# Kernel tuning notes

Measured on AMD Instinct MI355X. Metric: run time of the kernel, lower is better.

## Reference

```python
import jax, jax.numpy as jnp
import numpy as np
from jax import lax

X_SIZE, Z_SIZE, H, GC, PD = 256, 64, 64, 16, 2
B, K, T = 256, 16, 50
LOG_SIG_MIN, LOG_SIG_MAX, LOG_P_MAX = -10.0, 10.0, 50.0
ZX = X_SIZE + Z_SIZE
LSTM_IN = ZX + PD


def setup_inputs() -> dict:
    key = jax.random.key(0)
    ks = jax.random.split(key, 24)
    s = lambda fan_in: 1.0 / np.sqrt(fan_in)
    u = lambda k, shape, sc: jax.random.uniform(k, shape, jnp.float32, -sc, sc)
    inp = {
        'x': jax.random.normal(ks[0], (B, X_SIZE), jnp.float32),
        'z_stacked': jax.random.normal(ks[1], (K, B, Z_SIZE), jnp.float32),
        'input_seqs': jax.random.normal(ks[2], (B, 8, 2, 2, 6), jnp.float32),
        'pred_seqs': jax.random.normal(ks[3], (B, T, 2, 2, 6), jnp.float32),
        # initial_h / initial_c linears: ZX -> H
        'Wh0': u(ks[4], (H, ZX), s(ZX)), 'bh0': u(ks[5], (H,), s(ZX)),
        'Wc0': u(ks[6], (H, ZX), s(ZX)), 'bc0': u(ks[7], (H,), s(ZX)),
        # LSTMCell: gates order i,f,g,o
        'Wih': u(ks[8], (4 * H, LSTM_IN), s(H)), 'Whh': u(ks[9], (4 * H, H), s(H)),
        'bih': u(ks[10], (4 * H,), s(H)), 'bhh': u(ks[11], (4 * H,), s(H)),
        # GMM parameter heads: H -> GC / GC*PD
        'Wpi': u(ks[12], (GC, H), s(H)), 'bpi': u(ks[13], (GC,), s(H)),
        'Wmu': u(ks[14], (GC * PD, H), s(H)), 'bmu': u(ks[15], (GC * PD,), s(H)),
        'Wls': u(ks[16], (GC * PD, H), s(H)), 'bls': u(ks[17], (GC * PD,), s(H)),
        'Wcorr': u(ks[18], (GC, H), s(H)), 'bcorr': u(ks[19], (GC,), s(H)),
        'n_z_samples': K,
    }
    return inp


def _gmm2d_log_prob(log_pis, mus, log_sigmas, corrs, value):
    # log_pis/corrs: [K,B,T,GC]; mus/log_sigmas: [K,B,T,GC*PD]; value: [B,T,PD]
    ls = jnp.clip(log_sigmas, LOG_SIG_MIN, LOG_SIG_MAX).reshape(K, B, T, GC, PD)
    mu = mus.reshape(K, B, T, GC, PD)
    dx = value[None, :, :, None, :] - mu                      # [K,B,T,GC,PD]
    zscore = dx * jnp.exp(-ls)                                # dx / sigma
    one_m_rho2 = 1.0 - corrs ** 2
    quad = (zscore[..., 0] ** 2 + zscore[..., 1] ** 2
            - 2.0 * corrs * zscore[..., 0] * zscore[..., 1])
    comp = (-jnp.log(2.0 * jnp.pi) - ls.sum(-1)
            - 0.5 * jnp.log(one_m_rho2) - 0.5 * quad / one_m_rho2)
    log_pi_n = jax.nn.log_softmax(log_pis, axis=-1)
    log_p_t = jax.nn.logsumexp(log_pi_n + comp, axis=-1)      # [K,B,T]
    return jnp.minimum(log_p_t, LOG_P_MAX)


def reference(x, z_stacked, input_seqs, pred_seqs,
              Wh0, bh0, Wc0, bc0, Wih, Whh, bih, bhh,
              Wpi, bpi, Wmu, bmu, Wls, bls, Wcorr, bcorr, n_z_samples):
    tgt_future = pred_seqs[:, :, 1, 1, 2:4]                   # [B,T,2]
    tgt_present = input_seqs[:, -1, 1, 1, 2:4]                # [B,2]
    z = z_stacked.reshape(-1, z_stacked.shape[-1])            # [K*B, z]
    zx = jnp.concatenate([z, jnp.tile(x, (n_z_samples, 1))], axis=1)  # [N, ZX]
    N = zx.shape[0]
    h0 = zx @ Wh0.T + bh0
    c0 = zx @ Wc0.T + bc0
    decode_inputs = jnp.concatenate([tgt_present[:, None, :], tgt_future[:, :T - 1, :]], axis=1)  # [B,T,2]
    inputs = jnp.concatenate([
        jnp.broadcast_to(zx[:, None, :], (N, T, ZX)),
        jnp.tile(decode_inputs, (n_z_samples, 1, 1))], axis=2)  # [N,T,ZX+2]

    def step(carry, xt):
        h, c = carry
        gates = xt @ Wih.T + bih + h @ Whh.T + bhh
        i, f, g, o = jnp.split(gates, 4, axis=-1)
        c = jax.nn.sigmoid(f) * c + jax.nn.sigmoid(i) * jnp.tanh(g)
        h = jax.nn.sigmoid(o) * jnp.tanh(c)
        return (h, c), h

    _, hs = lax.scan(step, (h0, c0), jnp.swapaxes(inputs, 0, 1))  # [T,N,H]
    hs = jnp.swapaxes(hs, 0, 1)                                   # [N,T,H]

    log_pis = (hs @ Wpi.T + bpi).reshape(K, B, T, GC)
    mus = (hs @ Wmu.T + bmu).reshape(K, B, T, GC * PD)
    log_sigmas = (hs @ Wls.T + bls).reshape(K, B, T, GC * PD)
    corrs = jnp.tanh(hs @ Wcorr.T + bcorr).reshape(K, B, T, GC)

    log_p_yt_xz = _gmm2d_log_prob(log_pis, mus, log_sigmas, corrs, tgt_future)
    return log_p_yt_xz.sum(axis=2)                                # [K,B]
```

## Files before the change

### kernel.cpp

```cpp
#include <hip/hip_runtime.h>


#define T_ 50
#define SPB 16
#define ZXS 324
#define HFS 72
#define GLS 256
#define PLS 100

typedef __attribute__((ext_vector_type(8))) short short8;
typedef __attribute__((ext_vector_type(4))) float f32x4;

#define MFMA(a, b, c) __builtin_amdgcn_mfma_f32_16x16x32_bf16(a, b, c, 0, 0, 0)

__device__ __forceinline__ float sigf(float x)  { return 1.0f / (1.0f + __expf(-x)); }
__device__ __forceinline__ float tanh_(float x) { return 1.0f - 2.0f / (__expf(2.0f * x) + 1.0f); }

__device__ __forceinline__ void splitf(float f, unsigned short& hi, unsigned short& lo) {
    unsigned b = __float_as_uint(f);
    hi = (unsigned short)(b >> 16);
    float fh = __uint_as_float(b & 0xffff0000u);
    lo = (unsigned short)(__float_as_uint(f - fh) >> 16);
}

__device__ __forceinline__ void pack8(const float* p, short8& hi, short8& lo) {
    #pragma unroll
    for (int e = 0; e < 8; ++e) {
        unsigned short h, l;
        splitf(p[e], h, l);
        hi[e] = (short)h; lo[e] = (short)l;
    }
}

__launch_bounds__(512, 2)
__global__ void decoder_kernel(
    const float* __restrict__ x,       const float* __restrict__ z,
    const float* __restrict__ inp_seqs,const float* __restrict__ pred_seqs,
    const float* __restrict__ Wh0,     const float* __restrict__ bh0,
    const float* __restrict__ Wc0,     const float* __restrict__ bc0,
    const float* __restrict__ Wih,     const float* __restrict__ Whh,
    const float* __restrict__ bih,     const float* __restrict__ bhh,
    const float* __restrict__ Wpi,     const float* __restrict__ bpi,
    const float* __restrict__ Wmu,     const float* __restrict__ bmu,
    const float* __restrict__ Wls,     const float* __restrict__ bls,
    const float* __restrict__ Wcorr,   const float* __restrict__ bcorr,
    float* __restrict__ out)
{
    __shared__ __align__(16) float smem[9504];
    float* ZXL = smem;
    float* GL  = smem;
    float* PL  = smem + 4096;
    float* C0X = smem + 5696;
    unsigned short* HFhi = (unsigned short*)(smem + 6720);
    unsigned short* HFlo = (unsigned short*)(smem + 7296);
    float* FUT = smem + 7872;
    float* PRS = smem + 9472;

    const int j = threadIdx.x;
    const int w = j >> 6;
    const int l = j & 63;
    const int g = l >> 4;
    const int c = l & 15;
    const int blk = blockIdx.x;

    for (int e = j; e < SPB*320; e += 512) {
        int s = e / 320, k = e - s*320;
        int n = blk*SPB + s; int kk = n >> 8; int b = n & 255;
        ZXL[s*ZXS + k] = (k < 64) ? z[(kk*256 + b)*64 + k] : x[b*256 + (k - 64)];
    }
    for (int e = j; e < T_*SPB; e += 512) {
        int t = e >> 4, s = e & 15;
        int b = (blk*SPB + s) & 255;
        float2 v = *reinterpret_cast<const float2*>(pred_seqs + b*1200 + t*24 + 20);
        FUT[t*32 + s*2] = v.x; FUT[t*32 + s*2 + 1] = v.y;
    }
    if (j < SPB) {
        int b = (blk*SPB + j) & 255;
        float2 v = *reinterpret_cast<const float2*>(inp_seqs + b*192 + 188);
        PRS[j*2] = v.x; PRS[j*2 + 1] = v.y;
    }
    __syncthreads();

    const int gate0 = w*32 + c;
    const int gate1 = w*32 + 16 + c;
    const int colB  = w*16 + c;

    f32x4 gc0, gc1, accB;
    {
        float bA0 = bih[gate0] + bhh[gate0];
        float bA1 = bih[gate1] + bhh[gate1];
        float bB  = (w < 4) ? bh0[colB] : bc0[colB - 64];
        gc0 = (f32x4){bA0, bA0, bA0, bA0};
        gc1 = (f32x4){bA1, bA1, bA1, bA1};
        accB = (f32x4){bB, bB, bB, bB};
    }
    const float* rowA0 = Wih + gate0*322;
    const float* rowA1 = Wih + gate1*322;
    const float* rowB  = (w < 4) ? (Wh0 + colB*320) : (Wc0 + (colB - 64)*320);

    for (int ks = 0; ks < 10; ++ks) {
        int k0 = ks*32 + g*8;
        short8 ahi, alo, b0h, b0l, b1h, b1l, bbh, bbl;
        pack8(&ZXL[c*ZXS + k0], ahi, alo);
        pack8(rowA0 + k0, b0h, b0l);
        pack8(rowA1 + k0, b1h, b1l);
        pack8(rowB  + k0, bbh, bbl);
        gc0  = MFMA(ahi, b0h, gc0);  gc0  = MFMA(ahi, b0l, gc0);  gc0  = MFMA(alo, b0h, gc0);
        gc1  = MFMA(ahi, b1h, gc1);  gc1  = MFMA(ahi, b1l, gc1);  gc1  = MFMA(alo, b1h, gc1);
        accB = MFMA(ahi, bbh, accB); accB = MFMA(ahi, bbl, accB); accB = MFMA(alo, bbh, accB);
    }

    if (w < 4) {
        #pragma unroll
        for (int r = 0; r < 4; ++r) {
            int s = g*4 + r;
            unsigned short hh, ll; splitf(accB[r], hh, ll);
            HFhi[s*HFS + colB] = hh; HFlo[s*HFS + colB] = ll;
        }
    } else {
        #pragma unroll
        for (int r = 0; r < 4; ++r) C0X[(g*4 + r)*64 + (colB - 64)] = accB[r];
    }

    const float wd00 = rowA0[320], wd01 = rowA0[321];
    const float wd10 = rowA1[320], wd11 = rowA1[321];
    short8 w1h00, w1l00, w1h01, w1l01, w1h10, w1l10, w1h11, w1l11;
    pack8(Whh + gate0*64 +      g*8, w1h00, w1l00);
    pack8(Whh + gate0*64 + 32 + g*8, w1h01, w1l01);
    pack8(Whh + gate1*64 +      g*8, w1h10, w1l10);
    pack8(Whh + gate1*64 + 32 + g*8, w1h11, w1l11);

    short8 b3h0, b3l0, b3h1, b3l1;
    float bias3;
    {
        int r3 = (w < 6) ? (w*16 + c) : 0;
        const float* prow; float bb;
        if (r3 < 16)      { prow = Wpi   + r3*64;       bb = bpi[r3]; }
        else if (r3 < 48) { prow = Wmu   + (r3-16)*64;  bb = bmu[r3-16]; }
        else if (r3 < 80) { prow = Wls   + (r3-48)*64;  bb = bls[r3-48]; }
        else              { prow = Wcorr + (r3-80)*64;  bb = bcorr[r3-80]; }
        bias3 = bb;
        pack8(prow +      g*8, b3h0, b3l0);
        pack8(prow + 32 + g*8, b3h1, b3l1);
    }

    __syncthreads();

    const int u2 = j & 63, sg2 = j >> 6;
    float cst0 = C0X[(2*sg2 + 0)*64 + u2];
    float cst1 = C0X[(2*sg2 + 1)*64 + u2];

    const int s3 = j >> 4, g3 = j & 15;
    float sum = 0.0f;

    for (int t = 0; t < T_; ++t) {
        {
            const float* dptr = (t == 0) ? PRS : &FUT[(t-1)*32];
            f32x4 a0, a1;
            #pragma unroll
            for (int r = 0; r < 4; ++r) {
                float2 dv = *reinterpret_cast<const float2*>(dptr + (g*4 + r)*2);
                a0[r] = gc0[r] + dv.x*wd00 + dv.y*wd01;
                a1[r] = gc1[r] + dv.x*wd10 + dv.y*wd11;
            }
            short8 ah0 = *reinterpret_cast<const short8*>(HFhi + c*HFS +      g*8);
            short8 al0 = *reinterpret_cast<const short8*>(HFlo + c*HFS +      g*8);
            short8 ah1 = *reinterpret_cast<const short8*>(HFhi + c*HFS + 32 + g*8);
            short8 al1 = *reinterpret_cast<const short8*>(HFlo + c*HFS + 32 + g*8);
            a0 = MFMA(ah0, w1h00, a0); a0 = MFMA(ah0, w1l00, a0); a0 = MFMA(al0, w1h00, a0);
            a0 = MFMA(ah1, w1h01, a0); a0 = MFMA(ah1, w1l01, a0); a0 = MFMA(al1, w1h01, a0);
            a1 = MFMA(ah0, w1h10, a1); a1 = MFMA(ah0, w1l10, a1); a1 = MFMA(al0, w1h10, a1);
            a1 = MFMA(ah1, w1h11, a1); a1 = MFMA(ah1, w1l11, a1); a1 = MFMA(al1, w1h11, a1);
            #pragma unroll
            for (int r = 0; r < 4; ++r) {
                GL[(g*4 + r)*GLS + gate0] = a0[r];
                GL[(g*4 + r)*GLS + gate1] = a1[r];
            }
        }
        __syncthreads();

        {
            #pragma unroll
            for (int i = 0; i < 2; ++i) {
                int s = 2*sg2 + i;
                float gi = GL[s*GLS + u2];
                float gf = GL[s*GLS + 64  + u2];
                float gg = GL[s*GLS + 128 + u2];
                float go = GL[s*GLS + 192 + u2];
                float cp = (i == 0) ? cst0 : cst1;
                float cc = sigf(gf)*cp + sigf(gi)*tanh_(gg);
                if (i == 0) cst0 = cc; else cst1 = cc;
                float hh = sigf(go)*tanh_(cc);
                unsigned short uh, ul; splitf(hh, uh, ul);
                HFhi[s*HFS + u2] = uh; HFlo[s*HFS + u2] = ul;
            }
        }
        __syncthreads();

        if (w < 6) {
            short8 ah0 = *reinterpret_cast<const short8*>(HFhi + c*HFS +      g*8);
            short8 al0 = *reinterpret_cast<const short8*>(HFlo + c*HFS +      g*8);
            short8 ah1 = *reinterpret_cast<const short8*>(HFhi + c*HFS + 32 + g*8);
            short8 al1 = *reinterpret_cast<const short8*>(HFlo + c*HFS + 32 + g*8);
            f32x4 p = (f32x4){bias3, bias3, bias3, bias3};
            p = MFMA(ah0, b3h0, p); p = MFMA(ah0, b3l0, p); p = MFMA(al0, b3h0, p);
            p = MFMA(ah1, b3h1, p); p = MFMA(ah1, b3l1, p); p = MFMA(al1, b3h1, p);
            #pragma unroll
            for (int r = 0; r < 4; ++r) PL[(g*4 + r)*PLS + w*16 + c] = p[r];
        }
        __syncthreads();

        if (j < 256) {
            const float* pls = PL + s3*PLS;
            float a_pi = pls[g3];
            float a_m0 = pls[16 + 2*g3], a_m1 = pls[17 + 2*g3];
            float l0   = pls[48 + 2*g3], l1   = pls[49 + 2*g3];
            float a_co = pls[80 + g3];
            float v0 = FUT[t*32 + s3*2], v1 = FUT[t*32 + s3*2 + 1];
            l0 = fminf(fmaxf(l0, -10.0f), 10.0f);
            l1 = fminf(fmaxf(l1, -10.0f), 10.0f);
            float z0 = (v0 - a_m0) * __expf(-l0);
            float z1 = (v1 - a_m1) * __expf(-l1);
            float ct = tanh_(a_co);
            float omr = 1.0f - ct*ct;
            float quad = z0*z0 + z1*z1 - 2.0f*ct*z0*z1;
            float comp = -1.8378770664093453f - (l0 + l1) - 0.5f*__logf(omr) - 0.5f*quad/omr;
            float a = a_pi + comp;
            float m1v = a, m2v = a_pi;
            #pragma unroll
            for (int off = 1; off < 16; off <<= 1) {
                m1v = fmaxf(m1v, __shfl_xor(m1v, off));
                m2v = fmaxf(m2v, __shfl_xor(m2v, off));
            }
            float e1 = __expf(a - m1v), e2 = __expf(a_pi - m2v);
            #pragma unroll
            for (int off = 1; off < 16; off <<= 1) {
                e1 += __shfl_xor(e1, off);
                e2 += __shfl_xor(e2, off);
            }
            float logp = (m1v + __logf(e1)) - (m2v + __logf(e2));
            sum += fminf(logp, 50.0f);
        }
    }

    if (j < 256 && g3 == 0) out[blk*SPB + s3] = sum;
}

extern "C" void kernel_launch(void* const* d_in, const int* in_sizes, int n_in,
                              void* d_out, int out_size, void* d_ws, size_t ws_size,
                              hipStream_t stream) {
    const float* x     = (const float*)d_in[0];
    const float* z     = (const float*)d_in[1];
    const float* iseq  = (const float*)d_in[2];
    const float* pseq  = (const float*)d_in[3];
    const float* Wh0   = (const float*)d_in[4];
    const float* bh0   = (const float*)d_in[5];
    const float* Wc0   = (const float*)d_in[6];
    const float* bc0   = (const float*)d_in[7];
    const float* Wih   = (const float*)d_in[8];
    const float* Whh   = (const float*)d_in[9];
    const float* bih   = (const float*)d_in[10];
    const float* bhh   = (const float*)d_in[11];
    const float* Wpi   = (const float*)d_in[12];
    const float* bpi   = (const float*)d_in[13];
    const float* Wmu   = (const float*)d_in[14];
    const float* bmu   = (const float*)d_in[15];
    const float* Wls   = (const float*)d_in[16];
    const float* bls   = (const float*)d_in[17];
    const float* Wcorr = (const float*)d_in[18];
    const float* bcorr = (const float*)d_in[19];
    float* out = (float*)d_out;

    decoder_kernel<<<256, 512, 0, stream>>>(x, z, iseq, pseq, Wh0, bh0, Wc0, bc0,
                                            Wih, Whh, bih, bhh, Wpi, bpi, Wmu, bmu,
                                            Wls, bls, Wcorr, bcorr, out);
}
```

Measured before the change: 112.7 us.

## Restructure LSTM decoder: 8 samples per block, in-register gates, software-pipelined projection and GMM

Each block now handles 8 samples with 256 threads across 512 blocks, so more blocks run concurrently. Each wave computes all four gates for its hidden units in registers, which removes the gate round trip through shared memory and one barrier per step. The output projection and GMM stages are skewed by one and two timesteps, using double-buffered hidden-state and projection buffers, so each timestep needs a single barrier. The cost is more registers per thread, MFMAs on zero-padded rows (only 8 of 16 rows are valid), and extra drain steps after the loop.

```diff
diff --git a/kernel.cpp b/kernel.cpp
--- a/kernel.cpp
+++ b/kernel.cpp
@@ -2,10 +2,9 @@
 
 
 #define T_ 50
-#define SPB 16
+#define SPB 8
 #define ZXS 324
 #define HFS 72
-#define GLS 256
 #define PLS 100
 
 typedef __attribute__((ext_vector_type(8))) short short8;
@@ -32,7 +31,7 @@
     }
 }
 
-__launch_bounds__(512, 2)
+__launch_bounds__(256, 2)
 __global__ void decoder_kernel(
     const float* __restrict__ x,       const float* __restrict__ z,
     const float* __restrict__ inp_seqs,const float* __restrict__ pred_seqs,
@@ -46,15 +45,16 @@
     const float* __restrict__ Wcorr,   const float* __restrict__ bcorr,
     float* __restrict__ out)
 {
-    __shared__ __align__(16) float smem[9504];
+    __shared__ __align__(16) float smem[8320];
     float* ZXL = smem;
-    float* GL  = smem;
-    float* PL  = smem + 4096;
-    float* C0X = smem + 5696;
-    unsigned short* HFhi = (unsigned short*)(smem + 6720);
-    unsigned short* HFlo = (unsigned short*)(smem + 7296);
-    float* FUT = smem + 7872;
-    float* PRS = smem + 9472;
+    float* PL0 = smem;
+    float* PL1 = smem + 800;
+    unsigned short* HF0h = (unsigned short*)(smem + 5184);
+    unsigned short* HF0l = HF0h + 1152;
+    unsigned short* HF1h = HF0h + 2304;
+    unsigned short* HF1l = HF0h + 3456;
+    float* FUT = smem + 7488;
+    float* PRS = smem + 8288;
 
     const int j = threadIdx.x;
     const int w = j >> 6;
@@ -63,17 +63,23 @@
     const int c = l & 15;
     const int blk = blockIdx.x;
 
-    for (int e = j; e < SPB*320; e += 512) {
-        int s = e / 320, k = e - s*320;
-        int n = blk*SPB + s; int kk = n >> 8; int b = n & 255;
-        ZXL[s*ZXS + k] = (k < 64) ? z[(kk*256 + b)*64 + k] : x[b*256 + (k - 64)];
-    }
-    for (int e = j; e < T_*SPB; e += 512) {
-        int t = e >> 4, s = e & 15;
+    for (int e = j; e < 16*ZXS; e += 256) {
+        int s = e / ZXS, k = e - s*ZXS;
+        float v = 0.0f;
+        if (s < SPB && k < 320) {
+            int n = blk*SPB + s, kk = n >> 8, b = n & 255;
+            v = (k < 64) ? z[(kk*256 + b)*64 + k] : x[b*256 + (k - 64)];
+        }
+        ZXL[s*ZXS + k] = v;
+    }
+    for (int e = j; e < 2304; e += 256) smem[5184 + e] = 0.0f;
+    for (int e = j; e < T_*SPB; e += 256) {
+        int t = e >> 3, s = e & 7;
         int b = (blk*SPB + s) & 255;
         float2 v = *reinterpret_cast<const float2*>(pred_seqs + b*1200 + t*24 + 20);
-        FUT[t*32 + s*2] = v.x; FUT[t*32 + s*2 + 1] = v.y;
-    }
+        FUT[t*16 + s*2] = v.x; FUT[t*16 + s*2 + 1] = v.y;
+    }
+    if (j >= 16 && j < 32) PRS[j] = 0.0f;
     if (j < SPB) {
         int b = (blk*SPB + j) & 255;
         float2 v = *reinterpret_cast<const float2*>(inp_seqs + b*192 + 188);
@@ -81,169 +87,195 @@
     }
     __syncthreads();
 
-    const int gate0 = w*32 + c;
-    const int gate1 = w*32 + 16 + c;
-    const int colB  = w*16 + c;
-
-    f32x4 gc0, gc1, accB;
+    const int U  = 16*w + c;
+    const int R0 = U, R1 = 64 + U, R2 = 128 + U, R3 = 192 + U;
+
+    f32x4 gci, gcf, gcg, gco, h0a, c0a;
     {
-        float bA0 = bih[gate0] + bhh[gate0];
-        float bA1 = bih[gate1] + bhh[gate1];
-        float bB  = (w < 4) ? bh0[colB] : bc0[colB - 64];
-        gc0 = (f32x4){bA0, bA0, bA0, bA0};
-        gc1 = (f32x4){bA1, bA1, bA1, bA1};
-        accB = (f32x4){bB, bB, bB, bB};
-    }
-    const float* rowA0 = Wih + gate0*322;
-    const float* rowA1 = Wih + gate1*322;
-    const float* rowB  = (w < 4) ? (Wh0 + colB*320) : (Wc0 + (colB - 64)*320);
-
+        float bi_ = bih[R0] + bhh[R0], bf_ = bih[R1] + bhh[R1];
+        float bg_ = bih[R2] + bhh[R2], bo_ = bih[R3] + bhh[R3];
+        float bh_ = bh0[U], bc_ = bc0[U];
+        gci = (f32x4){bi_,bi_,bi_,bi_}; gcf = (f32x4){bf_,bf_,bf_,bf_};
+        gcg = (f32x4){bg_,bg_,bg_,bg_}; gco = (f32x4){bo_,bo_,bo_,bo_};
+        h0a = (f32x4){bh_,bh_,bh_,bh_}; c0a = (f32x4){bc_,bc_,bc_,bc_};
+    }
     for (int ks = 0; ks < 10; ++ks) {
         int k0 = ks*32 + g*8;
-        short8 ahi, alo, b0h, b0l, b1h, b1l, bbh, bbl;
-        pack8(&ZXL[c*ZXS + k0], ahi, alo);
-        pack8(rowA0 + k0, b0h, b0l);
-        pack8(rowA1 + k0, b1h, b1l);
-        pack8(rowB  + k0, bbh, bbl);
-        gc0  = MFMA(ahi, b0h, gc0);  gc0  = MFMA(ahi, b0l, gc0);  gc0  = MFMA(alo, b0h, gc0);
-        gc1  = MFMA(ahi, b1h, gc1);  gc1  = MFMA(ahi, b1l, gc1);  gc1  = MFMA(alo, b1h, gc1);
-        accB = MFMA(ahi, bbh, accB); accB = MFMA(ahi, bbl, accB); accB = MFMA(alo, bbh, accB);
-    }
-
-    if (w < 4) {
+        short8 ah, al, bh0_, bl0_, bh1_, bl1_, bh2_, bl2_, bh3_, bl3_, bhh_, bhl_, bch_, bcl_;
+        pack8(&ZXL[c*ZXS + k0], ah, al);
+        pack8(Wih + R0*322 + k0, bh0_, bl0_);
+        pack8(Wih + R1*322 + k0, bh1_, bl1_);
+        pack8(Wih + R2*322 + k0, bh2_, bl2_);
+        pack8(Wih + R3*322 + k0, bh3_, bl3_);
+        pack8(Wh0 + U*320 + k0, bhh_, bhl_);
+        pack8(Wc0 + U*320 + k0, bch_, bcl_);
+        gci = MFMA(ah, bh0_, gci); gci = MFMA(ah, bl0_, gci); gci = MFMA(al, bh0_, gci);
+        gcf = MFMA(ah, bh1_, gcf); gcf = MFMA(ah, bl1_, gcf); gcf = MFMA(al, bh1_, gcf);
+        gcg = MFMA(ah, bh2_, gcg); gcg = MFMA(ah, bl2_, gcg); gcg = MFMA(al, bh2_, gcg);
+        gco = MFMA(ah, bh3_, gco); gco = MFMA(ah, bl3_, gco); gco = MFMA(al, bh3_, gco);
+        h0a = MFMA(ah, bhh_, h0a); h0a = MFMA(ah, bhl_, h0a); h0a = MFMA(al, bhh_, h0a);
+        c0a = MFMA(ah, bch_, c0a); c0a = MFMA(ah, bcl_, c0a); c0a = MFMA(al, bch_, c0a);
+    }
+    float cst[4];
+    #pragma unroll
+    for (int r = 0; r < 4; ++r) {
+        cst[r] = c0a[r];
+        unsigned short hh, ll; splitf(h0a[r], hh, ll);
+        if (g < 2) {
+            HF0h[(4*g + r)*HFS + U] = hh;
+            HF0l[(4*g + r)*HFS + U] = ll;
+        }
+    }
+
+    const float wdi0 = Wih[R0*322+320], wdi1 = Wih[R0*322+321];
+    const float wdf0 = Wih[R1*322+320], wdf1 = Wih[R1*322+321];
+    const float wdg0 = Wih[R2*322+320], wdg1 = Wih[R2*322+321];
+    const float wdo0 = Wih[R3*322+320], wdo1 = Wih[R3*322+321];
+
+    short8 WIh0,WIl0,WIh1,WIl1, WFh0,WFl0,WFh1,WFl1, WGh0,WGl0,WGh1,WGl1, WOh0,WOl0,WOh1,WOl1;
+    pack8(Whh + R0*64 +      g*8, WIh0, WIl0); pack8(Whh + R0*64 + 32 + g*8, WIh1, WIl1);
+    pack8(Whh + R1*64 +      g*8, WFh0, WFl0); pack8(Whh + R1*64 + 32 + g*8, WFh1, WFl1);
+    pack8(Whh + R2*64 +      g*8, WGh0, WGl0); pack8(Whh + R2*64 + 32 + g*8, WGh1, WGl1);
+    pack8(Whh + R3*64 +      g*8, WOh0, WOl0); pack8(Whh + R3*64 + 32 + g*8, WOh1, WOl1);
+
+    auto projrow = [&](int r3, const float*& p, float& b) {
+        if      (r3 < 16) { p = Wpi   + r3*64;      b = bpi[r3]; }
+        else if (r3 < 48) { p = Wmu   + (r3-16)*64; b = bmu[r3-16]; }
+        else if (r3 < 80) { p = Wls   + (r3-48)*64; b = bls[r3-48]; }
+        else              { p = Wcorr + (r3-80)*64; b = bcorr[r3-80]; }
+    };
+    const int pt0 = w, pt1 = w + 4;
+    short8 q0h0,q0l0,q0h1,q0l1, q1h0={0},q1l0={0},q1h1={0},q1l1={0};
+    float bias3_0, bias3_1 = 0.0f;
+    {
+        const float* p; projrow(pt0*16 + c, p, bias3_0);
+        pack8(p +      g*8, q0h0, q0l0);
+        pack8(p + 32 + g*8, q0h1, q0l1);
+    }
+    if (w < 2) {
+        const float* p; projrow(pt1*16 + c, p, bias3_1);
+        pack8(p +      g*8, q1h0, q1l0);
+        pack8(p + 32 + g*8, q1h1, q1l1);
+    }
+
+    const int s3 = (j >> 4) & 7, g3 = j & 15;
+    float sum = 0.0f;
+
+    auto do_proj = [&](short8 ah0, short8 al0, short8 ah1, short8 al1, float* PLw) {
+        f32x4 p0 = (f32x4){bias3_0, bias3_0, bias3_0, bias3_0};
+        p0 = MFMA(ah0,q0h0,p0); p0 = MFMA(ah0,q0l0,p0); p0 = MFMA(al0,q0h0,p0);
+        p0 = MFMA(ah1,q0h1,p0); p0 = MFMA(ah1,q0l1,p0); p0 = MFMA(al1,q0h1,p0);
+        if (g < 2) {
+            #pragma unroll
+            for (int r = 0; r < 4; ++r) PLw[(4*g + r)*PLS + pt0*16 + c] = p0[r];
+        }
+        if (w < 2) {
+            f32x4 p1 = (f32x4){bias3_1, bias3_1, bias3_1, bias3_1};
+            p1 = MFMA(ah0,q1h0,p1); p1 = MFMA(ah0,q1l0,p1); p1 = MFMA(al0,q1h0,p1);
+            p1 = MFMA(ah1,q1h1,p1); p1 = MFMA(ah1,q1l1,p1); p1 = MFMA(al1,q1h1,p1);
+            if (g < 2) {
+                #pragma unroll
+                for (int r = 0; r < 4; ++r) PLw[(4*g + r)*PLS + pt1*16 + c] = p1[r];
+            }
+        }
+    };
+    auto do_gmm = [&](const float* pl, const float* fut2) {
+        const float* pls = pl + s3*PLS;
+        float a_pi = pls[g3];
+        float a_m0 = pls[16 + 2*g3], a_m1 = pls[17 + 2*g3];
+        float l0   = pls[48 + 2*g3], l1   = pls[49 + 2*g3];
+        float a_co = pls[80 + g3];
+        float v0 = fut2[s3*2], v1 = fut2[s3*2 + 1];
+        l0 = fminf(fmaxf(l0, -10.0f), 10.0f);
+        l1 = fminf(fmaxf(l1, -10.0f), 10.0f);
+        float z0 = (v0 - a_m0) * __expf(-l0);
+        float z1 = (v1 - a_m1) * __expf(-l1);
+        float ct = tanh_(a_co);
+        float omr = 1.0f - ct*ct;
+        float quad = z0*z0 + z1*z1 - 2.0f*ct*z0*z1;
+        float comp = -1.8378770664093453f - (l0 + l1) - 0.5f*__logf(omr) - 0.5f*quad/omr;
+        float a = a_pi + comp;
+        float m1v = a, m2v = a_pi;
+        #pragma unroll
+        for (int off = 1; off < 16; off <<= 1) {
+            m1v = fmaxf(m1v, __shfl_xor(m1v, off));
+            m2v = fmaxf(m2v, __shfl_xor(m2v, off));
+        }
+        float e1 = __expf(a - m1v), e2 = __expf(a_pi - m2v);
+        #pragma unroll
+        for (int off = 1; off < 16; off <<= 1) {
+            e1 += __shfl_xor(e1, off);
+            e2 += __shfl_xor(e2, off);
+        }
+        float logp = (m1v + __logf(e1)) - (m2v + __logf(e2));
+        sum += fminf(logp, 50.0f);
+    };
+
+    __syncthreads();
+
+    for (int t = 0; t < T_; ++t) {
+        const unsigned short* Hh = (t & 1) ? HF1h : HF0h;
+        const unsigned short* Hl = (t & 1) ? HF1l : HF0l;
+        unsigned short* Nh = (t & 1) ? HF0h : HF1h;
+        unsigned short* Nl = (t & 1) ? HF0l : HF1l;
+        float* PLw = (t & 1) ? PL1 : PL0;
+        const float* PLr = (t & 1) ? PL0 : PL1;
+
+        short8 ah0 = *reinterpret_cast<const short8*>(Hh + c*HFS +      g*8);
+        short8 al0 = *reinterpret_cast<const short8*>(Hl + c*HFS +      g*8);
+        short8 ah1 = *reinterpret_cast<const short8*>(Hh + c*HFS + 32 + g*8);
+        short8 al1 = *reinterpret_cast<const short8*>(Hl + c*HFS + 32 + g*8);
+
+        const float* dptr = (t == 0) ? PRS : (FUT + (t-1)*16);
+        f32x4 ai, af, ag, ao;
         #pragma unroll
         for (int r = 0; r < 4; ++r) {
-            int s = g*4 + r;
-            unsigned short hh, ll; splitf(accB[r], hh, ll);
-            HFhi[s*HFS + colB] = hh; HFlo[s*HFS + colB] = ll;
-        }
-    } else {
+            float2 dv = *reinterpret_cast<const float2*>(dptr + (4*g + r)*2);
+            ai[r] = gci[r] + dv.x*wdi0 + dv.y*wdi1;
+            af[r] = gcf[r] + dv.x*wdf0 + dv.y*wdf1;
+            ag[r] = gcg[r] + dv.x*wdg0 + dv.y*wdg1;
+            ao[r] = gco[r] + dv.x*wdo0 + dv.y*wdo1;
+        }
+        ai = MFMA(ah0,WIh0,ai); ai = MFMA(ah0,WIl0,ai); ai = MFMA(al0,WIh0,ai);
+        ai = MFMA(ah1,WIh1,ai); ai = MFMA(ah1,WIl1,ai); ai = MFMA(al1,WIh1,ai);
+        af = MFMA(ah0,WFh0,af); af = MFMA(ah0,WFl0,af); af = MFMA(al0,WFh0,af);
+        af = MFMA(ah1,WFh1,af); af = MFMA(ah1,WFl1,af); af = MFMA(al1,WFh1,af);
+        ag = MFMA(ah0,WGh0,ag); ag = MFMA(ah0,WGl0,ag); ag = MFMA(al0,WGh0,ag);
+        ag = MFMA(ah1,WGh1,ag); ag = MFMA(ah1,WGl1,ag); ag = MFMA(al1,WGh1,ag);
+        ao = MFMA(ah0,WOh0,ao); ao = MFMA(ah0,WOl0,ao); ao = MFMA(al0,WOh0,ao);
+        ao = MFMA(ah1,WOh1,ao); ao = MFMA(ah1,WOl1,ao); ao = MFMA(al1,WOh1,ao);
+
+        if (t >= 1) do_proj(ah0, al0, ah1, al1, PLw);
+
         #pragma unroll
-        for (int r = 0; r < 4; ++r) C0X[(g*4 + r)*64 + (colB - 64)] = accB[r];
-    }
-
-    const float wd00 = rowA0[320], wd01 = rowA0[321];
-    const float wd10 = rowA1[320], wd11 = rowA1[321];
-    short8 w1h00, w1l00, w1h01, w1l01, w1h10, w1l10, w1h11, w1l11;
-    pack8(Whh + gate0*64 +      g*8, w1h00, w1l00);
-    pack8(Whh + gate0*64 + 32 + g*8, w1h01, w1l01);
-    pack8(Whh + gate1*64 +      g*8, w1h10, w1l10);
-    pack8(Whh + gate1*64 + 32 + g*8, w1h11, w1l11);
-
-    short8 b3h0, b3l0, b3h1, b3l1;
-    float bias3;
+        for (int r = 0; r < 4; ++r) {
+            float cc = sigf(af[r])*cst[r] + sigf(ai[r])*tanh_(ag[r]);
+            cst[r] = cc;
+            float hv = sigf(ao[r])*tanh_(cc);
+            unsigned short hh, ll; splitf(hv, hh, ll);
+            if (g < 2) {
+                Nh[(4*g + r)*HFS + U] = hh;
+                Nl[(4*g + r)*HFS + U] = ll;
+            }
+        }
+
+        if (t >= 2 && j < 128) do_gmm(PLr, FUT + (t-2)*16);
+
+        __syncthreads();
+    }
+
     {
-        int r3 = (w < 6) ? (w*16 + c) : 0;
-        const float* prow; float bb;
-        if (r3 < 16)      { prow = Wpi   + r3*64;       bb = bpi[r3]; }
-        else if (r3 < 48) { prow = Wmu   + (r3-16)*64;  bb = bmu[r3-16]; }
-        else if (r3 < 80) { prow = Wls   + (r3-48)*64;  bb = bls[r3-48]; }
-        else              { prow = Wcorr + (r3-80)*64;  bb = bcorr[r3-80]; }
-        bias3 = bb;
-        pack8(prow +      g*8, b3h0, b3l0);
-        pack8(prow + 32 + g*8, b3h1, b3l1);
-    }
-
-    __syncthreads();
-
-    const int u2 = j & 63, sg2 = j >> 6;
-    float cst0 = C0X[(2*sg2 + 0)*64 + u2];
-    float cst1 = C0X[(2*sg2 + 1)*64 + u2];
-
-    const int s3 = j >> 4, g3 = j & 15;
-    float sum = 0.0f;
-
-    for (int t = 0; t < T_; ++t) {
-        {
-            const float* dptr = (t == 0) ? PRS : &FUT[(t-1)*32];
-            f32x4 a0, a1;
-            #pragma unroll
-            for (int r = 0; r < 4; ++r) {
-                float2 dv = *reinterpret_cast<const float2*>(dptr + (g*4 + r)*2);
-                a0[r] = gc0[r] + dv.x*wd00 + dv.y*wd01;
-                a1[r] = gc1[r] + dv.x*wd10 + dv.y*wd11;
-            }
-            short8 ah0 = *reinterpret_cast<const short8*>(HFhi + c*HFS +      g*8);
-            short8 al0 = *reinterpret_cast<const short8*>(HFlo + c*HFS +      g*8);
-            short8 ah1 = *reinterpret_cast<const short8*>(HFhi + c*HFS + 32 + g*8);
-            short8 al1 = *reinterpret_cast<const short8*>(HFlo + c*HFS + 32 + g*8);
-            a0 = MFMA(ah0, w1h00, a0); a0 = MFMA(ah0, w1l00, a0); a0 = MFMA(al0, w1h00, a0);
-            a0 = MFMA(ah1, w1h01, a0); a0 = MFMA(ah1, w1l01, a0); a0 = MFMA(al1, w1h01, a0);
-            a1 = MFMA(ah0, w1h10, a1); a1 = MFMA(ah0, w1l10, a1); a1 = MFMA(al0, w1h10, a1);
-            a1 = MFMA(ah1, w1h11, a1); a1 = MFMA(ah1, w1l11, a1); a1 = MFMA(al1, w1h11, a1);
-            #pragma unroll
-            for (int r = 0; r < 4; ++r) {
-                GL[(g*4 + r)*GLS + gate0] = a0[r];
-                GL[(g*4 + r)*GLS + gate1] = a1[r];
-            }
-        }
+        short8 ah0 = *reinterpret_cast<const short8*>(HF0h + c*HFS +      g*8);
+        short8 al0 = *reinterpret_cast<const short8*>(HF0l + c*HFS +      g*8);
+        short8 ah1 = *reinterpret_cast<const short8*>(HF0h + c*HFS + 32 + g*8);
+        short8 al1 = *reinterpret_cast<const short8*>(HF0l + c*HFS + 32 + g*8);
+        do_proj(ah0, al0, ah1, al1, PL0);
+        if (j < 128) do_gmm(PL1, FUT + 48*16);
         __syncthreads();
-
-        {
-            #pragma unroll
-            for (int i = 0; i < 2; ++i) {
-                int s = 2*sg2 + i;
-                float gi = GL[s*GLS + u2];
-                float gf = GL[s*GLS + 64  + u2];
-                float gg = GL[s*GLS + 128 + u2];
-                float go = GL[s*GLS + 192 + u2];
-                float cp = (i == 0) ? cst0 : cst1;
-                float cc = sigf(gf)*cp + sigf(gi)*tanh_(gg);
-                if (i == 0) cst0 = cc; else cst1 = cc;
-                float hh = sigf(go)*tanh_(cc);
-                unsigned short uh, ul; splitf(hh, uh, ul);
-                HFhi[s*HFS + u2] = uh; HFlo[s*HFS + u2] = ul;
-            }
-        }
-        __syncthreads();
-
-        if (w < 6) {
-            short8 ah0 = *reinterpret_cast<const short8*>(HFhi + c*HFS +      g*8);
-            short8 al0 = *reinterpret_cast<const short8*>(HFlo + c*HFS +      g*8);
-            short8 ah1 = *reinterpret_cast<const short8*>(HFhi + c*HFS + 32 + g*8);
-            short8 al1 = *reinterpret_cast<const short8*>(HFlo + c*HFS + 32 + g*8);
-            f32x4 p = (f32x4){bias3, bias3, bias3, bias3};
-            p = MFMA(ah0, b3h0, p); p = MFMA(ah0, b3l0, p); p = MFMA(al0, b3h0, p);
-            p = MFMA(ah1, b3h1, p); p = MFMA(ah1, b3l1, p); p = MFMA(al1, b3h1, p);
-            #pragma unroll
-            for (int r = 0; r < 4; ++r) PL[(g*4 + r)*PLS + w*16 + c] = p[r];
-        }
-        __syncthreads();
-
-        if (j < 256) {
-            const float* pls = PL + s3*PLS;
-            float a_pi = pls[g3];
-            float a_m0 = pls[16 + 2*g3], a_m1 = pls[17 + 2*g3];
-            float l0   = pls[48 + 2*g3], l1   = pls[49 + 2*g3];
-            float a_co = pls[80 + g3];
-            float v0 = FUT[t*32 + s3*2], v1 = FUT[t*32 + s3*2 + 1];
-            l0 = fminf(fmaxf(l0, -10.0f), 10.0f);
-            l1 = fminf(fmaxf(l1, -10.0f), 10.0f);
-            float z0 = (v0 - a_m0) * __expf(-l0);
-            float z1 = (v1 - a_m1) * __expf(-l1);
-            float ct = tanh_(a_co);
-            float omr = 1.0f - ct*ct;
-            float quad = z0*z0 + z1*z1 - 2.0f*ct*z0*z1;
-            float comp = -1.8378770664093453f - (l0 + l1) - 0.5f*__logf(omr) - 0.5f*quad/omr;
-            float a = a_pi + comp;
-            float m1v = a, m2v = a_pi;
-            #pragma unroll
-            for (int off = 1; off < 16; off <<= 1) {
-                m1v = fmaxf(m1v, __shfl_xor(m1v, off));
-                m2v = fmaxf(m2v, __shfl_xor(m2v, off));
-            }
-            float e1 = __expf(a - m1v), e2 = __expf(a_pi - m2v);
-            #pragma unroll
-            for (int off = 1; off < 16; off <<= 1) {
-                e1 += __shfl_xor(e1, off);
-                e2 += __shfl_xor(e2, off);
-            }
-            float logp = (m1v + __logf(e1)) - (m2v + __logf(e2));
-            sum += fminf(logp, 50.0f);
-        }
-    }
-
-    if (j < 256 && g3 == 0) out[blk*SPB + s3] = sum;
+        if (j < 128) do_gmm(PL0, FUT + 49*16);
+    }
+
+    if (j < 128 && g3 == 0) out[blk*SPB + s3] = sum;
 }
 
 extern "C" void kernel_launch(void* const* d_in, const int* in_sizes, int n_in,
@@ -271,7 +303,7 @@
     const float* bcorr = (const float*)d_in[19];
     float* out = (float*)d_out;
 
-    decoder_kernel<<<256, 512, 0, stream>>>(x, z, iseq, pseq, Wh0, bh0, Wc0, bc0,
+    decoder_kernel<<<512, 256, 0, stream>>>(x, z, iseq, pseq, Wh0, bh0, Wc0, bc0,
                                             Wih, Whh, bih, bhh, Wpi, bpi, Wmu, bmu,
                                             Wls, bls, Wcorr, bcorr, out);
 }
```

Measured after the change: 158.4 us. 1.4x slower.
